# Performance work log

Hardware: AMD Instinct MI355X
Metric: run time of the kernel (lower is better)

Reference implementation:

```python
import jax, jax.numpy as jnp
import numpy as np

B, S, V, P = 16, 100, 50000, 45
WE, PE, H = 100, 50, 400
H2 = 2 * H  # bilstm output size


def _lstm(x, Wih, Whh, b):
    """Unidirectional LSTM over time. x: [B,S,D] -> h: [B,S,H]. PyTorch gate order i,f,g,o."""
    Hs = Whh.shape[1]
    def step(carry, xt):
        h, c = carry
        g = xt @ Wih.T + h @ Whh.T + b
        i, f, gg, o = jnp.split(g, 4, axis=-1)
        c = jax.nn.sigmoid(f) * c + jax.nn.sigmoid(i) * jnp.tanh(gg)
        h = jax.nn.sigmoid(o) * jnp.tanh(c)
        return (h, c), h
    Bn = x.shape[0]
    init = (jnp.zeros((Bn, Hs), x.dtype), jnp.zeros((Bn, Hs), x.dtype))
    _, hs = jax.lax.scan(step, init, jnp.swapaxes(x, 0, 1))
    return jnp.swapaxes(hs, 0, 1)


def _bilstm_layer(x, Wf_ih, Wf_hh, bf, Wb_ih, Wb_hh, bb):
    hf = _lstm(x, Wf_ih, Wf_hh, bf)
    hb = _lstm(x[:, ::-1, :], Wb_ih, Wb_hh, bb)[:, ::-1, :]
    return jnp.concatenate([hf, hb], axis=-1)


def setup_inputs() -> dict:
    key = jax.random.key(0)
    ks = jax.random.split(key, 24)
    def n(k, shape, s=0.1):
        return jax.random.normal(k, shape, jnp.float32) * s
    inp = {
        "input_tokens": jax.random.randint(ks[0], (B, S), 0, V),
        "input_pos": jax.random.randint(ks[1], (B, S), 0, P),
        "input_head": jax.random.randint(ks[2], (B, S), 0, S),
        "word_W": n(ks[3], (V, WE)),
        "pos_W": n(ks[4], (P, PE)),
        "l0f_Wih": n(ks[5], (4 * H, WE + PE)), "l0f_Whh": n(ks[6], (4 * H, H)), "l0f_b": n(ks[7], (4 * H,)),
        "l0b_Wih": n(ks[8], (4 * H, WE + PE)), "l0b_Whh": n(ks[9], (4 * H, H)), "l0b_b": n(ks[10], (4 * H,)),
        "l1f_Wih": n(ks[11], (4 * H, H2)), "l1f_Whh": n(ks[12], (4 * H, H)), "l1f_b": n(ks[13], (4 * H,)),
        "l1b_Wih": n(ks[14], (4 * H, H2)), "l1b_Whh": n(ks[15], (4 * H, H)), "l1b_b": n(ks[16], (4 * H,)),
        "ua_W": n(ks[17], (H2, H2)), "ua_b": n(ks[18], (H2,)),
        "wa_W": n(ks[19], (H2, H2)), "wa_b": n(ks[20], (H2,)),
        "va_W": n(ks[21], (H2,)),
    }
    return inp


def reference(input_tokens, input_pos, input_head, word_W, pos_W,
              l0f_Wih, l0f_Whh, l0f_b, l0b_Wih, l0b_Whh, l0b_b,
              l1f_Wih, l1f_Whh, l1f_b, l1b_Wih, l1b_Whh, l1b_b,
              ua_W, ua_b, wa_W, wa_b, va_W):
    # embeddings (dropout is identity at eval)
    x = jnp.concatenate([word_W[input_tokens], pos_W[input_pos]], axis=-1)  # [B,S,150]
    h1 = _bilstm_layer(x, l0f_Wih, l0f_Whh, l0f_b, l0b_Wih, l0b_Whh, l0b_b)   # [B,S,H2]
    out = _bilstm_layer(h1, l1f_Wih, l1f_Whh, l1f_b, l1b_Wih, l1b_Whh, l1b_b)  # [B,S,H2]

    # batched additive biaffine scoring for targets i = 1..S-1 over all source positions j
    ua = out @ ua_W.T + ua_b  # u_a(source)  [B,S,H2]
    wa = out @ wa_W.T + wa_b  # w_a(target)  [B,S,H2]
    # g[b,t,j] = v_a . tanh(ua[b,j] + wa[b,t+1])
    g = jnp.einsum('btjh,h->btj', jnp.tanh(ua[:, None, :, :] + wa[:, 1:, None, :]), va_W)  # [B,S-1,S]
    # mask: output[:, j, 0] == output[:, i, 0]  (masks self, matching torch's output.eq(target)[:,:,0])
    mask = out[:, 1:, 0][:, :, None] == out[:, :, 0][:, None, :]  # [B,S-1,S]
    g = jnp.where(mask, -10000.0, g)
    logp = jax.nn.log_softmax(g, axis=2)  # log_softmax over source positions (torch dim=1)

    # loss: sum over i of NLLLoss(mean over batch, ignore_index=-1)
    gold = input_head[:, 1:]  # [B,S-1]
    valid = (gold != -1)
    nll = -jnp.take_along_axis(logp, jnp.clip(gold, 0, S - 1)[:, :, None], axis=2)[..., 0]
    nll = nll * valid.astype(logp.dtype)
    denom = jnp.maximum(valid.sum(axis=0), 1).astype(logp.dtype)
    loss = jnp.sum(nll.sum(axis=0) / denom)

    parent_prob_table = jnp.exp(logp)  # [B,S-1,S]
    preds = jnp.argmax(parent_prob_table, axis=2)  # [B,S-1]
    return (loss, preds, parent_prob_table)
```

## Files before the change

### kernel.cpp

```cpp
#include <hip/hip_runtime.h>

#define BB 16
#define SS 100
#define HH 400
#define H2 800
#define G4 1600
#define DIN0 150
#define KP0 160

#define OFF_GF   240000ULL
#define OFF_GB   2800000ULL
#define OFF_H1   5360000ULL
#define OFF_OUT2 6640000ULL
#define OFF_NLL  8078400ULL
#define OFF_EXH  8081600ULL
#define EX_U16_PER_PLANE 1331200ULL

typedef _Float16 f16x8 __attribute__((ext_vector_type(8)));
typedef float    f32x4 __attribute__((ext_vector_type(4)));
typedef unsigned long long u64x2 __attribute__((ext_vector_type(2)));

static __device__ __forceinline__ unsigned chkp(unsigned long long q) {
    return ((unsigned)q == 0xFFFFFFFFu) | ((unsigned)(q >> 32) == 0xFFFFFFFFu);
}
static __device__ __forceinline__ unsigned long long sanq(unsigned long long q) {
    if ((unsigned)q == 0xFFFFFFFFu)         q &= 0xFFFFFFFF00000000ull;
    if ((unsigned)(q >> 32) == 0xFFFFFFFFu) q &= 0x00000000FFFFFFFFull;
    return q;
}

static __device__ __forceinline__ void cvt8(const float* v, f16x8& hi, f16x8& lo)
{
#pragma unroll
    for (int i = 0; i < 8; i++) {
        _Float16 h = (_Float16)v[i];
        hi[i] = h;
        lo[i] = (_Float16)((v[i] - (float)h) * 2048.f);
    }
}
static __device__ __forceinline__ void cvt_pair8(float4 a, float4 b,
                                                 f16x8& hi, f16x8& lo)
{
    float v[8] = {a.x, a.y, a.z, a.w, b.x, b.y, b.z, b.w};
    cvt8(v, hi, lo);
}

__global__ __launch_bounds__(256) void gemm_l0_embed_dual(
    const int* __restrict__ tok, const int* __restrict__ pos,
    const float* __restrict__ wW, const float* __restrict__ pW,
    const float* __restrict__ W0, const float* __restrict__ b0, float* __restrict__ C0,
    const float* __restrict__ W1, const float* __restrict__ b1, float* __restrict__ C1,
    unsigned int* __restrict__ poison, int poison_words)
{
    {
        int nthreads = gridDim.x * gridDim.y * 256;
        int gtid = (blockIdx.y * gridDim.x + blockIdx.x) * 256 + threadIdx.x;
        for (int i = gtid; i < poison_words; i += nthreads) poison[i] = 0xFFFFFFFFu;
    }

    int half = gridDim.x >> 1;
    int sel = blockIdx.x >= half;
    int bx = blockIdx.x - (sel ? half : 0);
    const float* W = sel ? W1 : W0;
    const float* bias = sel ? b1 : b0;
    float* C = sel ? C1 : C0;

    int tid = threadIdx.x;
    int wv = tid >> 6, l = tid & 63;
    int lm = l & 15, lk = l >> 4;
    int rs = bx * 64 + wv * 16;
    int n0 = blockIdx.y * 64;

    int trow[4], prow[4];
#pragma unroll
    for (int ct = 0; ct < 4; ct++) {
        int r = n0 + ct * 16 + lm;
        trow[ct] = tok[r];
        prow[ct] = pos[r];
    }
    const float* wrow = W + (size_t)(rs + lm) * DIN0;

    f32x4 accH[4], accX[4];
#pragma unroll
    for (int ct = 0; ct < 4; ct++) {
        accH[ct] = {0.f, 0.f, 0.f, 0.f};
        accX[ct] = {0.f, 0.f, 0.f, 0.f};
    }

#pragma unroll
    for (int kt = 0; kt < 5; kt++) {
        int kb = kt << 5;
        float wv8[8];
#pragma unroll
        for (int e = 0; e < 8; e++) {
            int k = kb + lk * 8 + e;
            wv8[e] = (k < DIN0) ? wrow[k] : 0.f;
        }
        f16x8 wh, wl;
        cvt8(wv8, wh, wl);
#pragma unroll
        for (int ct = 0; ct < 4; ct++) {
            float av8[8];
#pragma unroll
            for (int e = 0; e < 8; e++) {
                int k = kb + lk * 8 + e;
                float v = 0.f;
                if (k < 100)       v = wW[trow[ct] * 100 + k];
                else if (k < DIN0) v = pW[prow[ct] * 50 + (k - 100)];
                av8[e] = v;
            }
            f16x8 ah, al;
            cvt8(av8, ah, al);
            accH[ct] = __builtin_amdgcn_mfma_f32_16x16x32_f16(wh, ah, accH[ct], 0, 0, 0);
            accX[ct] = __builtin_amdgcn_mfma_f32_16x16x32_f16(wh, al, accX[ct], 0, 0, 0);
            accX[ct] = __builtin_amdgcn_mfma_f32_16x16x32_f16(wl, ah, accX[ct], 0, 0, 0);
        }
    }

    float4 bv = *(const float4*)&bias[rs + lk * 4];
#pragma unroll
    for (int ct = 0; ct < 4; ct++) {
        f32x4 v = accH[ct] + accX[ct] * (1.f / 2048.f);
        float4 o;
        o.x = v[0] + bv.x; o.y = v[1] + bv.y; o.z = v[2] + bv.z; o.w = v[3] + bv.w;
        *(float4*)&C[(size_t)(n0 + ct * 16 + lm) * G4 + rs + lk * 4] = o;
    }
}

__global__ __launch_bounds__(256) void gemm_nt_mfma_dual(
    const float* __restrict__ A,
    const float* __restrict__ W0, const float* __restrict__ b0, float* __restrict__ C0,
    const float* __restrict__ W1, const float* __restrict__ b1, float* __restrict__ C1,
    int N, int K, int R,
    unsigned int* __restrict__ poison, int poison_words)
{
    if (poison) {
        int nthreads = gridDim.x * gridDim.y * 256;
        int gtid = (blockIdx.y * gridDim.x + blockIdx.x) * 256 + threadIdx.x;
        for (int i = gtid; i < poison_words; i += nthreads) poison[i] = 0xFFFFFFFFu;
    }

    int half = gridDim.x >> 1;
    int sel = blockIdx.x >= half;
    int bx = blockIdx.x - (sel ? half : 0);
    const float* W = sel ? W1 : W0;
    const float* bias = sel ? b1 : b0;
    float* C = sel ? C1 : C0;

    int tid = threadIdx.x;
    int wv = tid >> 6, l = tid & 63;
    int lm = l & 15, lk = l >> 4;
    int rs = bx * 64 + wv * 16;
    if (rs >= R) return;
    int n0 = blockIdx.y * 64;

    const float* wrow = W + (size_t)(rs + lm) * K + lk * 8;
    const float* arow = A + (size_t)(n0 + lm) * K + lk * 8;

    f32x4 accH[4], accX[4];
#pragma unroll
    for (int ct = 0; ct < 4; ct++) {
        accH[ct] = {0.f, 0.f, 0.f, 0.f};
        accX[ct] = {0.f, 0.f, 0.f, 0.f};
    }

    int ksteps = K >> 5;
    for (int kt = 0; kt < ksteps; kt++) {
        int kb = kt << 5;
        float4 wlo4 = *(const float4*)(wrow + kb);
        float4 whi4 = *(const float4*)(wrow + kb + 4);
        f16x8 wh, wl;
        cvt_pair8(wlo4, whi4, wh, wl);
#pragma unroll
        for (int ct = 0; ct < 4; ct++) {
            const float* ap = arow + (size_t)(ct * 16) * K + kb;
            float4 aa = *(const float4*)ap;
            float4 ab = *(const float4*)(ap + 4);
            f16x8 ah, al;
            cvt_pair8(aa, ab, ah, al);
            accH[ct] = __builtin_amdgcn_mfma_f32_16x16x32_f16(wh, ah, accH[ct], 0, 0, 0);
            accX[ct] = __builtin_amdgcn_mfma_f32_16x16x32_f16(wh, al, accX[ct], 0, 0, 0);
            accX[ct] = __builtin_amdgcn_mfma_f32_16x16x32_f16(wl, ah, accX[ct], 0, 0, 0);
        }
    }

    float4 bv = *(const float4*)&bias[rs + lk * 4];
#pragma unroll
    for (int ct = 0; ct < 4; ct++) {
        f32x4 v = accH[ct] + accX[ct] * (1.f / 2048.f);
        float4 o;
        o.x = v[0] + bv.x; o.y = v[1] + bv.y; o.z = v[2] + bv.z; o.w = v[3] + bv.w;
        *(float4*)&C[(size_t)(n0 + ct * 16 + lm) * R + rs + lk * 4] = o;
    }
}

__global__ __launch_bounds__(64, 1) void lstm_layer_kernel(
    const float* __restrict__ Gf, const float* __restrict__ Gb,
    const float* __restrict__ Wf, const float* __restrict__ Wb,
    float* __restrict__ hbuf,
    unsigned short* __restrict__ exhi,
    unsigned short* __restrict__ exlo)
{
    const int dir = blockIdx.x / 100;
    const int wg  = blockIdx.x % 100;
    const int j0  = wg * 4;
    const float* __restrict__ G = dir ? Gb : Gf;
    const float* __restrict__ W = dir ? Wb : Wf;

    const int l   = threadIdx.x;
    const int b   = l & 15;
    const int hi4 = l >> 4;

    __shared__ __attribute__((aligned(16))) unsigned short ahi[13 * 64 * 8];
    __shared__ __attribute__((aligned(16))) unsigned short alo[13 * 64 * 8];
    __shared__ float gl[16 * 17];

    {
        const int m = b;
        const int g = m >> 2, jj = m & 3;
        const float* wrow = W + (size_t)(g * HH + j0 + jj) * HH;
        for (int kt = 0; kt < 13; kt++) {
            for (int e = 0; e < 8; e++) {
                int k = kt * 32 + hi4 * 8 + e;
                float w = (k < HH) ? wrow[k] : 0.f;
                _Float16 wh = (_Float16)w;
                _Float16 wl = (_Float16)((w - (float)wh) * 2048.f);
                ahi[(kt * 64 + l) * 8 + e] = __builtin_bit_cast(unsigned short, wh);
                alo[(kt * 64 + l) * 8 + e] = __builtin_bit_cast(unsigned short, wl);
            }
        }
    }
    __syncthreads();

    float c_reg = 0.f;
    unsigned short* exh_d = exhi + (size_t)dir * 100 * 13 * 512;
    unsigned short* exl_d = exlo + (size_t)dir * 100 * 13 * 512;
    const int pad_lane = (hi4 >= 2);

    for (int s = 0; s < SS; s++) {
        const int time = dir ? (SS - 1 - s) : s;
        f32x4 gpre = *(const f32x4*)&G[(size_t)(b * SS + time) * G4 + hi4 * HH + j0];

        f32x4 acc;
        if (s > 0) {
            const unsigned long long* pbh =
                (const unsigned long long*)(exh_d + (size_t)(s - 1) * 13 * 512);
            const unsigned long long* pbl =
                (const unsigned long long*)(exl_d + (size_t)(s - 1) * 13 * 512);
            u64x2 vh2[13], vl2[13];
            vh2[12] = {0ull, 0ull};
            vl2[12] = {0ull, 0ull};
            unsigned bad = 1;
            for (int guard = 0; guard < (1 << 13); guard++) {
                bad = 0;
#pragma unroll
                for (int kt = 0; kt < 12; kt++) {
                    size_t q = (size_t)(kt * 64 + l) * 2;
                    vh2[kt][0] = __hip_atomic_load(pbh + q,     __ATOMIC_RELAXED, __HIP_MEMORY_SCOPE_AGENT);
                    vh2[kt][1] = __hip_atomic_load(pbh + q + 1, __ATOMIC_RELAXED, __HIP_MEMORY_SCOPE_AGENT);
                    vl2[kt][0] = __hip_atomic_load(pbl + q,     __ATOMIC_RELAXED, __HIP_MEMORY_SCOPE_AGENT);
                    vl2[kt][1] = __hip_atomic_load(pbl + q + 1, __ATOMIC_RELAXED, __HIP_MEMORY_SCOPE_AGENT);
                }
                if (!pad_lane) {
                    size_t q = (size_t)(12 * 64 + l) * 2;
                    vh2[12][0] = __hip_atomic_load(pbh + q,     __ATOMIC_RELAXED, __HIP_MEMORY_SCOPE_AGENT);
                    vh2[12][1] = __hip_atomic_load(pbh + q + 1, __ATOMIC_RELAXED, __HIP_MEMORY_SCOPE_AGENT);
                    vl2[12][0] = __hip_atomic_load(pbl + q,     __ATOMIC_RELAXED, __HIP_MEMORY_SCOPE_AGENT);
                    vl2[12][1] = __hip_atomic_load(pbl + q + 1, __ATOMIC_RELAXED, __HIP_MEMORY_SCOPE_AGENT);
                    bad |= chkp(vh2[12][0]) | chkp(vh2[12][1])
                         | chkp(vl2[12][0]) | chkp(vl2[12][1]);
                }
#pragma unroll
                for (int kt = 0; kt < 12; kt++) {
                    bad |= chkp(vh2[kt][0]) | chkp(vh2[kt][1])
                         | chkp(vl2[kt][0]) | chkp(vl2[kt][1]);
                }
                if (__ballot(bad != 0) == 0ull) break;
                __builtin_amdgcn_s_sleep(2);
            }
            if (bad) {
#pragma unroll
                for (int kt = 0; kt < 13; kt++) {
                    vh2[kt][0] = sanq(vh2[kt][0]); vh2[kt][1] = sanq(vh2[kt][1]);
                    vl2[kt][0] = sanq(vl2[kt][0]); vl2[kt][1] = sanq(vl2[kt][1]);
                }
            }
            asm volatile("" ::: "memory");

            f32x4 aHH = gpre;
            f32x4 aHL = {0.f, 0.f, 0.f, 0.f};
            f32x4 aLH = {0.f, 0.f, 0.f, 0.f};
#pragma unroll
            for (int kt = 0; kt < 13; kt++) {
                f16x8 bhv = __builtin_bit_cast(f16x8, vh2[kt]);
                f16x8 blv = __builtin_bit_cast(f16x8, vl2[kt]);
                f16x8 wh = *(const f16x8*)&ahi[(kt * 64 + l) * 8];
                f16x8 wl = *(const f16x8*)&alo[(kt * 64 + l) * 8];
                aHH = __builtin_amdgcn_mfma_f32_16x16x32_f16(wh, bhv, aHH, 0, 0, 0);
                aHL = __builtin_amdgcn_mfma_f32_16x16x32_f16(wh, blv, aHL, 0, 0, 0);
                aLH = __builtin_amdgcn_mfma_f32_16x16x32_f16(wl, bhv, aLH, 0, 0, 0);
            }
            acc = aHH + (aHL + aLH) * (1.f / 2048.f);
        } else {
            acc = gpre;
        }

#pragma unroll
        for (int q = 0; q < 4; q++) gl[(4 * hi4 + q) * 17 + b] = acc[q];
        __syncthreads();

        const int jj = hi4;
        float gi = gl[( 0 + jj) * 17 + b];
        float gf = gl[( 4 + jj) * 17 + b];
        float gg = gl[( 8 + jj) * 17 + b];
        float go = gl[(12 + jj) * 17 + b];
        __syncthreads();

        float si = 1.f / (1.f + expf(-gi));
        float sf = 1.f / (1.f + expf(-gf));
        float tg = tanhf(gg);
        float so = 1.f / (1.f + expf(-go));
        float c  = sf * c_reg + si * tg;
        c_reg = c;
        float h  = so * tanhf(c);

        if (s < SS - 1) {
            _Float16 hh = (_Float16)h;
            _Float16 hl = (_Float16)((h - (float)hh) * 2048.f);
            unsigned uh = __builtin_bit_cast(unsigned short, hh);
            unsigned ul = __builtin_bit_cast(unsigned short, hl);
            unsigned ph = uh | (((unsigned)__shfl_down((int)uh, 16)) << 16);
            unsigned pl = ul | (((unsigned)__shfl_down((int)ul, 16)) << 16);
            if ((jj & 1) == 0) {
                int k0 = j0 + jj;
                int kt = k0 >> 5, ko = k0 & 31;
                int lg = ko >> 3, e = ko & 7;
                size_t u16idx = ((size_t)(s * 13 + kt) * 64 + (lg * 16 + b)) * 8 + e;
                __hip_atomic_store((unsigned*)(exh_d + u16idx), ph,
                                   __ATOMIC_RELAXED, __HIP_MEMORY_SCOPE_AGENT);
                __hip_atomic_store((unsigned*)(exl_d + u16idx), pl,
                                   __ATOMIC_RELAXED, __HIP_MEMORY_SCOPE_AGENT);
            }
        }

        hbuf[(size_t)(b * SS + time) * H2 + dir * HH + j0 + jj] = h;
    }
}

#define ITILE 11
__global__ __launch_bounds__(256) void attn_scores_softmax_kernel(
    const float* __restrict__ ua, const float* __restrict__ wa,
    const float* __restrict__ va, const float* __restrict__ out2,
    const int* __restrict__ head, float* __restrict__ outb,
    float* __restrict__ nll)
{
    int b  = blockIdx.x / 9;
    int i0 = (blockIdx.x % 9) * ITILE;
    int tid = threadIdx.x;
    __shared__ float ua_t[100][101];
    __shared__ float wa_t[ITILE][102];
    __shared__ float sacc[ITILE][101];
    __shared__ float va_t[100];
    __shared__ float h0[100];

    for (int p = tid; p < ITILE * 101; p += 256) ((float*)sacc)[p] = 0.f;
    if (tid < 100) h0[tid] = out2[(size_t)(b * SS + tid) * H2];

    for (int ht = 0; ht < 8; ht++) {
        int hh0 = ht * 100;
        __syncthreads();
        for (int p = tid; p < 100 * 100; p += 256) {
            int j = p / 100, hh = p % 100;
            ua_t[j][hh] = ua[(size_t)(b * SS + j) * H2 + hh0 + hh];
        }
        for (int p = tid; p < ITILE * 100; p += 256) {
            int il = p / 100, hh = p % 100;
            wa_t[il][hh] = wa[(size_t)(b * SS + i0 + il + 1) * H2 + hh0 + hh];
        }
        if (tid < 100) va_t[tid] = va[hh0 + tid];
        __syncthreads();
        for (int p = tid; p < ITILE * 100; p += 256) {
            int il = p / 100, j = p % 100;
            float acc = 0.f;
#pragma unroll 4
            for (int hh = 0; hh < 100; hh++) {
                float x = ua_t[j][hh] + wa_t[il][hh];
                float z = __expf(2.f * x);
                float th = 1.f - 2.f * __builtin_amdgcn_rcpf(z + 1.f);
                acc = fmaf(th, va_t[hh], acc);
            }
            sacc[il][j] += acc;
        }
    }
    __syncthreads();

    int wv = tid >> 6, ln = tid & 63;
    for (int il = wv; il < ITILE; il += 4) {
        int i = i0 + il;
        int bi = b * 99 + i;
        float h_t = h0[i + 1];
        int j1 = ln, j2 = ln + 64;
        float s1 = sacc[il][j1];
        if (h0[j1] == h_t) s1 = -10000.0f;
        float s2 = -1e30f;
        if (j2 < 100) {
            s2 = sacc[il][j2];
            if (h0[j2] == h_t) s2 = -10000.0f;
        }
        float v = s1; int vi = j1;
        if (s2 > v) { v = s2; vi = j2; }
        for (int k = 32; k >= 1; k >>= 1) {
            float vo = __shfl_xor(v, k);
            int   io = __shfl_xor(vi, k);
            if (vo > v || (vo == v && io < vi)) { v = vo; vi = io; }
        }
        float m = v; int amax = vi;
        float e1 = __expf(s1 - m);
        float e2 = (j2 < 100) ? __expf(s2 - m) : 0.f;
        float sum = e1 + e2;
        for (int k = 32; k >= 1; k >>= 1) sum += __shfl_xor(sum, k);
        float inv = 1.f / sum;
        outb[1 + 1584 + (size_t)bi * 100 + j1] = e1 * inv;
        if (j2 < 100) outb[1 + 1584 + (size_t)bi * 100 + j2] = e2 * inv;
        if (ln == 0) {
            outb[1 + bi] = (float)amax;
            int gold = head[b * SS + i + 1];
            bool valid = (gold != -1);
            int gc = gold < 0 ? 0 : (gold > 99 ? 99 : gold);
            float sgc = sacc[il][gc];
            if (h0[gc] == h_t) sgc = -10000.0f;
            nll[bi] = valid ? -(sgc - m - logf(sum)) : 0.f;
        }
    }
}

__global__ __launch_bounds__(128) void loss_kernel(
    const float* __restrict__ nll, const int* __restrict__ head,
    float* __restrict__ outb)
{
    __shared__ float red[128];
    int tid = threadIdx.x;
    float contrib = 0.f;
    if (tid < 99) {
        int i = tid;
        float tot = 0.f; int cv = 0;
        for (int b = 0; b < BB; b++) {
            tot += nll[b * 99 + i];
            cv += (head[b * SS + i + 1] != -1) ? 1 : 0;
        }
        int denom = cv > 0 ? cv : 1;
        contrib = tot / (float)denom;
    }
    red[tid] = contrib;
    __syncthreads();
    for (int off = 64; off >= 1; off >>= 1) {
        if (tid < off) red[tid] += red[tid + off];
        __syncthreads();
    }
    if (tid == 0) outb[0] = red[0];
}

extern "C" void kernel_launch(void* const* d_in, const int* in_sizes, int n_in,
                              void* d_out, int out_size, void* d_ws, size_t ws_size,
                              hipStream_t stream) {
    const int*   tok     = (const int*)d_in[0];
    const int*   pos     = (const int*)d_in[1];
    const int*   head    = (const int*)d_in[2];
    const float* word_W  = (const float*)d_in[3];
    const float* pos_W   = (const float*)d_in[4];
    const float* l0f_Wih = (const float*)d_in[5];
    const float* l0f_Whh = (const float*)d_in[6];
    const float* l0f_b   = (const float*)d_in[7];
    const float* l0b_Wih = (const float*)d_in[8];
    const float* l0b_Whh = (const float*)d_in[9];
    const float* l0b_b   = (const float*)d_in[10];
    const float* l1f_Wih = (const float*)d_in[11];
    const float* l1f_Whh = (const float*)d_in[12];
    const float* l1f_b   = (const float*)d_in[13];
    const float* l1b_Wih = (const float*)d_in[14];
    const float* l1b_Whh = (const float*)d_in[15];
    const float* l1b_b   = (const float*)d_in[16];
    const float* ua_W    = (const float*)d_in[17];
    const float* ua_b    = (const float*)d_in[18];
    const float* wa_W    = (const float*)d_in[19];
    const float* wa_b    = (const float*)d_in[20];
    const float* va_W    = (const float*)d_in[21];

    float* ws   = (float*)d_ws;
    float* gf   = ws + OFF_GF;
    float* gb   = ws + OFF_GB;
    float* h1   = ws + OFF_H1;
    float* out2 = ws + OFF_OUT2;
    float* nllb = ws + OFF_NLL;
    unsigned short* exhi = (unsigned short*)(ws + OFF_EXH);
    unsigned short* exlo = exhi + EX_U16_PER_PLANE;
    float* outf = (float*)d_out;

    gemm_l0_embed_dual<<<dim3(50, 25), 256, 0, stream>>>(
        tok, pos, word_W, pos_W,
        l0f_Wih, l0f_b, gf, l0b_Wih, l0b_b, gb,
        (unsigned int*)exhi, (int)EX_U16_PER_PLANE);
    lstm_layer_kernel<<<dim3(200), 64, 0, stream>>>(
        gf, gb, l0f_Whh, l0b_Whh, h1, exhi, exlo);
    gemm_nt_mfma_dual<<<dim3(50, 25), 256, 0, stream>>>(
        h1, l1f_Wih, l1f_b, gf, l1b_Wih, l1b_b, gb, 1600, H2, G4,
        (unsigned int*)exhi, (int)EX_U16_PER_PLANE);
    lstm_layer_kernel<<<dim3(200), 64, 0, stream>>>(
        gf, gb, l1f_Whh, l1b_Whh, out2, exhi, exlo);
    gemm_nt_mfma_dual<<<dim3(26, 25), 256, 0, stream>>>(
        out2, ua_W, ua_b, gf, wa_W, wa_b, gb, 1600, H2, H2, nullptr, 0);
    attn_scores_softmax_kernel<<<dim3(16 * 9), 256, 0, stream>>>(
        gf, gb, va_W, out2, head, outf, nllb);
    loss_kernel<<<dim3(1), 128, 0, stream>>>(nllb, head, outf);
}
```

Baseline: 1.435 ms.

## Stage activation tiles in shared memory with double buffering in input GEMMs

Both input-projection GEMM kernels now load each 64x32 activation tile once per block, convert it to the fp16 hi/lo split once, and store it in double-buffered LDS, where all four wavefronts read it. Previously every wavefront loaded and converted the same activation rows itself. The next tile's global loads are issued before the current tile's MFMAs, which overlaps load latency with compute. The cost is a __syncthreads per k-step and extra LDS traffic. Wavefronts past the edge of R now stay in the loop to take part in the barriers instead of returning early.

```diff
diff --git a/kernel.cpp b/kernel.cpp
--- a/kernel.cpp
+++ b/kernel.cpp
@@ -45,6 +45,8 @@
     cvt8(v, hi, lo);
 }
 
+#define AROW 40
+
 __global__ __launch_bounds__(256) void gemm_l0_embed_dual(
     const int* __restrict__ tok, const int* __restrict__ pos,
     const float* __restrict__ wW, const float* __restrict__ pW,
@@ -71,13 +73,12 @@
     int rs = bx * 64 + wv * 16;
     int n0 = blockIdx.y * 64;
 
-    int trow[4], prow[4];
-#pragma unroll
-    for (int ct = 0; ct < 4; ct++) {
-        int r = n0 + ct * 16 + lm;
-        trow[ct] = tok[r];
-        prow[ct] = pos[r];
-    }
+    __shared__ __attribute__((aligned(16))) unsigned short AhiS[2][64 * AROW];
+    __shared__ __attribute__((aligned(16))) unsigned short AloS[2][64 * AROW];
+
+    int sr = tid >> 2, sc = (tid & 3) * 8;
+    int t_ = tok[n0 + sr], p_ = pos[n0 + sr];
+
     const float* wrow = W + (size_t)(rs + lm) * DIN0;
 
     f32x4 accH[4], accX[4];
@@ -87,33 +88,60 @@
         accX[ct] = {0.f, 0.f, 0.f, 0.f};
     }
 
-#pragma unroll
-    for (int kt = 0; kt < 5; kt++) {
-        int kb = kt << 5;
-        float wv8[8];
-#pragma unroll
-        for (int e = 0; e < 8; e++) {
-            int k = kb + lk * 8 + e;
-            wv8[e] = (k < DIN0) ? wrow[k] : 0.f;
-        }
-        f16x8 wh, wl;
-        cvt8(wv8, wh, wl);
-#pragma unroll
-        for (int ct = 0; ct < 4; ct++) {
-            float av8[8];
+    float a8[8];
+#pragma unroll
+    for (int e = 0; e < 8; e++) {
+        int k = sc + e;
+        a8[e] = (k < 100) ? wW[t_ * 100 + k]
+              : (k < DIN0) ? pW[p_ * 50 + (k - 100)] : 0.f;
+    }
+    float w8[8];
+#pragma unroll
+    for (int e = 0; e < 8; e++) {
+        int k = lk * 8 + e;
+        w8[e] = (k < DIN0) ? wrow[k] : 0.f;
+    }
+    {
+        f16x8 h, lo2; cvt8(a8, h, lo2);
+        *(f16x8*)&AhiS[0][sr * AROW + sc] = h;
+        *(f16x8*)&AloS[0][sr * AROW + sc] = lo2;
+    }
+
+    const int nkt = 5;
+    for (int kt = 0; kt < nkt; kt++) {
+        __syncthreads();
+        bool more = (kt + 1 < nkt);
+        float a8n[8], w8n[8];
+        if (more) {
+            int kb = (kt + 1) << 5;
+#pragma unroll
+            for (int e = 0; e < 8; e++) {
+                int k = kb + sc + e;
+                a8n[e] = (k < 100) ? wW[t_ * 100 + k]
+                       : (k < DIN0) ? pW[p_ * 50 + (k - 100)] : 0.f;
+            }
 #pragma unroll
             for (int e = 0; e < 8; e++) {
                 int k = kb + lk * 8 + e;
-                float v = 0.f;
-                if (k < 100)       v = wW[trow[ct] * 100 + k];
-                else if (k < DIN0) v = pW[prow[ct] * 50 + (k - 100)];
-                av8[e] = v;
-            }
-            f16x8 ah, al;
-            cvt8(av8, ah, al);
+                w8n[e] = (k < DIN0) ? wrow[k] : 0.f;
+            }
+        }
+        f16x8 wh, wl; cvt8(w8, wh, wl);
+        int buf = kt & 1;
+#pragma unroll
+        for (int ct = 0; ct < 4; ct++) {
+            f16x8 ah = *(const f16x8*)&AhiS[buf][(ct * 16 + lm) * AROW + lk * 8];
+            f16x8 al = *(const f16x8*)&AloS[buf][(ct * 16 + lm) * AROW + lk * 8];
             accH[ct] = __builtin_amdgcn_mfma_f32_16x16x32_f16(wh, ah, accH[ct], 0, 0, 0);
             accX[ct] = __builtin_amdgcn_mfma_f32_16x16x32_f16(wh, al, accX[ct], 0, 0, 0);
             accX[ct] = __builtin_amdgcn_mfma_f32_16x16x32_f16(wl, ah, accX[ct], 0, 0, 0);
+        }
+        if (more) {
+            f16x8 h, lo2; cvt8(a8n, h, lo2);
+            *(f16x8*)&AhiS[buf ^ 1][sr * AROW + sc] = h;
+            *(f16x8*)&AloS[buf ^ 1][sr * AROW + sc] = lo2;
+#pragma unroll
+            for (int e = 0; e < 8; e++) w8[e] = w8n[e];
         }
     }
 
@@ -131,7 +159,7 @@
     const float* __restrict__ A,
     const float* __restrict__ W0, const float* __restrict__ b0, float* __restrict__ C0,
     const float* __restrict__ W1, const float* __restrict__ b1, float* __restrict__ C1,
-    int N, int K, int R,
+    int K, int R,
     unsigned int* __restrict__ poison, int poison_words)
 {
     if (poison) {
@@ -151,11 +179,15 @@
     int wv = tid >> 6, l = tid & 63;
     int lm = l & 15, lk = l >> 4;
     int rs = bx * 64 + wv * 16;
-    if (rs >= R) return;
+    bool active = (rs < R);
     int n0 = blockIdx.y * 64;
 
-    const float* wrow = W + (size_t)(rs + lm) * K + lk * 8;
-    const float* arow = A + (size_t)(n0 + lm) * K + lk * 8;
+    __shared__ __attribute__((aligned(16))) unsigned short AhiS[2][64 * AROW];
+    __shared__ __attribute__((aligned(16))) unsigned short AloS[2][64 * AROW];
+
+    int sr = tid >> 2, sc = (tid & 3) * 8;
+    const float* arow_g = A + (size_t)(n0 + sr) * K + sc;
+    const float* wrow = W + (size_t)((active ? rs : 0) + lm) * K + lk * 8;
 
     f32x4 accH[4], accX[4];
 #pragma unroll
@@ -164,26 +196,52 @@
         accX[ct] = {0.f, 0.f, 0.f, 0.f};
     }
 
-    int ksteps = K >> 5;
-    for (int kt = 0; kt < ksteps; kt++) {
-        int kb = kt << 5;
-        float4 wlo4 = *(const float4*)(wrow + kb);
-        float4 whi4 = *(const float4*)(wrow + kb + 4);
-        f16x8 wh, wl;
-        cvt_pair8(wlo4, whi4, wh, wl);
-#pragma unroll
-        for (int ct = 0; ct < 4; ct++) {
-            const float* ap = arow + (size_t)(ct * 16) * K + kb;
-            float4 aa = *(const float4*)ap;
-            float4 ab = *(const float4*)(ap + 4);
-            f16x8 ah, al;
-            cvt_pair8(aa, ab, ah, al);
-            accH[ct] = __builtin_amdgcn_mfma_f32_16x16x32_f16(wh, ah, accH[ct], 0, 0, 0);
-            accX[ct] = __builtin_amdgcn_mfma_f32_16x16x32_f16(wh, al, accX[ct], 0, 0, 0);
-            accX[ct] = __builtin_amdgcn_mfma_f32_16x16x32_f16(wl, ah, accX[ct], 0, 0, 0);
-        }
-    }
-
+    float a8[8];
+    *(float4*)a8       = *(const float4*)arow_g;
+    *(float4*)(a8 + 4) = *(const float4*)(arow_g + 4);
+    float4 wA = {0,0,0,0}, wB = {0,0,0,0};
+    if (active) { wA = *(const float4*)wrow; wB = *(const float4*)(wrow + 4); }
+    {
+        f16x8 h, lo2; cvt8(a8, h, lo2);
+        *(f16x8*)&AhiS[0][sr * AROW + sc] = h;
+        *(f16x8*)&AloS[0][sr * AROW + sc] = lo2;
+    }
+
+    int nkt = K >> 5;
+    for (int kt = 0; kt < nkt; kt++) {
+        __syncthreads();
+        bool more = (kt + 1 < nkt);
+        float a8n[8]; float4 wAn = {0,0,0,0}, wBn = {0,0,0,0};
+        if (more) {
+            int kb = (kt + 1) << 5;
+            *(float4*)a8n       = *(const float4*)(arow_g + kb);
+            *(float4*)(a8n + 4) = *(const float4*)(arow_g + kb + 4);
+            if (active) {
+                wAn = *(const float4*)(wrow + kb);
+                wBn = *(const float4*)(wrow + kb + 4);
+            }
+        }
+        if (active) {
+            f16x8 wh, wl; cvt_pair8(wA, wB, wh, wl);
+            int buf = kt & 1;
+#pragma unroll
+            for (int ct = 0; ct < 4; ct++) {
+                f16x8 ah = *(const f16x8*)&AhiS[buf][(ct * 16 + lm) * AROW + lk * 8];
+                f16x8 al = *(const f16x8*)&AloS[buf][(ct * 16 + lm) * AROW + lk * 8];
+                accH[ct] = __builtin_amdgcn_mfma_f32_16x16x32_f16(wh, ah, accH[ct], 0, 0, 0);
+                accX[ct] = __builtin_amdgcn_mfma_f32_16x16x32_f16(wh, al, accX[ct], 0, 0, 0);
+                accX[ct] = __builtin_amdgcn_mfma_f32_16x16x32_f16(wl, ah, accX[ct], 0, 0, 0);
+            }
+        }
+        if (more) {
+            f16x8 h, lo2; cvt8(a8n, h, lo2);
+            *(f16x8*)&AhiS[(kt & 1) ^ 1][sr * AROW + sc] = h;
+            *(f16x8*)&AloS[(kt & 1) ^ 1][sr * AROW + sc] = lo2;
+            wA = wAn; wB = wBn;
+        }
+    }
+
+    if (!active) return;
     float4 bv = *(const float4*)&bias[rs + lk * 4];
 #pragma unroll
     for (int ct = 0; ct < 4; ct++) {
@@ -503,12 +561,12 @@
     lstm_layer_kernel<<<dim3(200), 64, 0, stream>>>(
         gf, gb, l0f_Whh, l0b_Whh, h1, exhi, exlo);
     gemm_nt_mfma_dual<<<dim3(50, 25), 256, 0, stream>>>(
-        h1, l1f_Wih, l1f_b, gf, l1b_Wih, l1b_b, gb, 1600, H2, G4,
+        h1, l1f_Wih, l1f_b, gf, l1b_Wih, l1b_b, gb, H2, G4,
         (unsigned int*)exhi, (int)EX_U16_PER_PLANE);
     lstm_layer_kernel<<<dim3(200), 64, 0, stream>>>(
         gf, gb, l1f_Whh, l1b_Whh, out2, exhi, exlo);
     gemm_nt_mfma_dual<<<dim3(26, 25), 256, 0, stream>>>(
-        out2, ua_W, ua_b, gf, wa_W, wa_b, gb, 1600, H2, H2, nullptr, 0);
+        out2, ua_W, ua_b, gf, wa_W, wa_b, gb, H2, H2, nullptr, 0);
     attn_scores_softmax_kernel<<<dim3(16 * 9), 256, 0, stream>>>(
         gf, gb, va_W, out2, head, outf, nllb);
     loss_kernel<<<dim3(1), 128, 0, stream>>>(nllb, head, outf);
```

Measured after the change: 1.276 ms. -11.1%, faster.
